# Optimization experiments

Measured on AMD Instinct MI355X. Metric: run time of the kernel, lower is better.

The kernel has to match this reference:

```python
import jax, jax.numpy as jnp
import numpy as np

B, N, C = 2, 2048, 2048
H, KV = 16, 4          # query heads, kv heads
D = C // H             # head_dim = 128
ROPE_BASE = 10000.0


def rope_cos_sin(position_ids, dim):
    # interleaved RoPE: freqs for even indices, repeated pairwise to full dim
    inv_freq = 1.0 / (ROPE_BASE ** (jnp.arange(0, dim, 2, dtype=jnp.float32) / dim))
    ang = position_ids[..., None].astype(jnp.float32) * inv_freq   # [B, N, D/2]
    cos = jnp.repeat(jnp.cos(ang), 2, axis=-1)                     # [B, N, D]
    sin = jnp.repeat(jnp.sin(ang), 2, axis=-1)
    return cos, sin


def rotate_half_interleaved(x):
    # (x0, x1, x2, x3, ...) -> (-x1, x0, -x3, x2, ...)
    x1 = x[..., 0::2]
    x2 = x[..., 1::2]
    return jnp.stack([-x2, x1], axis=-1).reshape(x.shape)


def apply_rotary(x, cos, sin):
    # x: [B, h, N, D]; cos/sin: [B, N, D]
    return x * cos[:, None] + rotate_half_interleaved(x) * sin[:, None]


def setup_inputs() -> dict:
    key = jax.random.key(0)
    ks = jax.random.split(key, 5)
    s = 0.02
    return dict(
        x=jax.random.normal(ks[0], (B, N, C), jnp.float32),
        position_ids=jnp.tile(jnp.arange(N, dtype=jnp.int32), (B, 1)),
        Wq=jax.random.normal(ks[1], (C, C), jnp.float32) * s,
        bq=jnp.zeros((C,), jnp.float32),
        Wk=jax.random.normal(ks[2], (C, KV * D), jnp.float32) * s,
        bk=jnp.zeros((KV * D,), jnp.float32),
        Wv=jax.random.normal(ks[3], (C, KV * D), jnp.float32) * s,
        bv=jnp.zeros((KV * D,), jnp.float32),
        Wo=jax.random.normal(ks[4], (C, C), jnp.float32) * s,
    )


def reference(x, position_ids, Wq, bq, Wk, bk, Wv, bv, Wo):
    Bx, Nx, Cx = x.shape
    q = (x @ Wq + bq).reshape(Bx, Nx, H, D).transpose(0, 2, 1, 3)   # [B,H,N,D]
    k = (x @ Wk + bk).reshape(Bx, Nx, KV, D).transpose(0, 2, 1, 3)  # [B,KV,N,D]
    v = (x @ Wv + bv).reshape(Bx, Nx, KV, D).transpose(0, 2, 1, 3)

    cos, sin = rope_cos_sin(position_ids, D)
    q = apply_rotary(q, cos, sin)
    k = apply_rotary(k, cos, sin)

    # GQA expand: head h uses kv head h // groups (matches unsqueeze+expand+reshape)
    groups = H // KV
    k = jnp.repeat(k, groups, axis=1)   # [B,H,N,D]
    v = jnp.repeat(v, groups, axis=1)

    attn = jnp.einsum('bhqd,bhkd->bhqk', q, k) * (D ** -0.5)        # [B,H,N,N]
    causal_mask = jnp.triu(jnp.ones((Nx, Nx), dtype=bool), 1)
    attn = jnp.where(causal_mask, -jnp.inf, attn)
    attn = jax.nn.softmax(attn, axis=-1)

    out = jnp.einsum('bhqk,bhkd->bhqd', attn, v)
    out = out.transpose(0, 2, 1, 3).reshape(Bx, Nx, Cx)
    return out @ Wo
```

## Files before the change

kernel.cpp:

```cpp
#include <hip/hip_runtime.h>
#include <cstdint>
#include <type_traits>

typedef unsigned short u16;
typedef unsigned int u32;
typedef __bf16 bf16x8 __attribute__((ext_vector_type(8)));
typedef float f32x4 __attribute__((ext_vector_type(4)));

constexpr int BB = 2;
constexpr int SEQ = 2048;
constexpr int CH = 2048;
constexpr int NH = 16;
constexpr int NKV = 4;
constexpr int HD = 128;
constexpr int QKVC = CH + 2 * NKV * HD;

#define DI __device__ __forceinline__

DI u16 f2b(float x) {
  u32 u = __float_as_uint(x);
  u = u + 0x7FFFu + ((u >> 16) & 1u);
  return (u16)(u >> 16);
}
DI float b2f(u16 u) { return __uint_as_float(((u32)u) << 16); }

DI u32 pack2bf(float lo, float hi) {
  return __builtin_amdgcn_perm(__float_as_uint(hi), __float_as_uint(lo), 0x07060302u);
}

DI void glds16(const void* g, void* l) {
  __builtin_amdgcn_global_load_lds(
      (__attribute__((address_space(1))) void*)(uintptr_t)g,
      (__attribute__((address_space(3))) void*)(u32)(uintptr_t)l, 16, 0, 0);
}

__global__ __launch_bounds__(256) void xconv_kernel(const float* __restrict__ in,
                                                    u16* __restrict__ out, int n4) {
  int i = blockIdx.x * 256 + threadIdx.x;
  if (i < n4) {
    float4 v = *(const float4*)&in[(size_t)i * 4];
    ushort4 o;
    o.x = f2b(v.x); o.y = f2b(v.y); o.z = f2b(v.z); o.w = f2b(v.w);
    *(ushort4*)&out[(size_t)i * 4] = o;
  }
}

__global__ __launch_bounds__(256) void wtrans4_kernel(
    const float* __restrict__ Wq, const float* __restrict__ Wk,
    const float* __restrict__ Wv, const float* __restrict__ Wo,
    u16* __restrict__ wqkvt, u16* __restrict__ wot) {
  const int z = blockIdx.z;
  const float* in;
  u16* out;
  int Cc;
  if (z == 0)      { in = Wq; out = wqkvt;                                Cc = CH; }
  else if (z == 1) { in = Wk; out = wqkvt + (size_t)CH * CH;              Cc = NKV * HD; }
  else if (z == 2) { in = Wv; out = wqkvt + (size_t)(CH + NKV * HD) * CH; Cc = NKV * HD; }
  else             { in = Wo; out = wot;                                  Cc = CH; }
  if ((int)blockIdx.y * 64 >= Cc) return;

  __shared__ u16 tile[64 * 65];
  const int r0 = blockIdx.x * 64, c0 = blockIdx.y * 64;
  const int tid = threadIdx.x;
  for (int c = tid; c < 1024; c += 256) {
    int r = c >> 4, col = (c & 15) * 4;
    float4 v = *(const float4*)&in[(size_t)(r0 + r) * Cc + c0 + col];
    tile[r * 65 + col + 0] = f2b(v.x);
    tile[r * 65 + col + 1] = f2b(v.y);
    tile[r * 65 + col + 2] = f2b(v.z);
    tile[r * 65 + col + 3] = f2b(v.w);
  }
  __syncthreads();
  for (int c = tid; c < 1024; c += 256) {
    int r = c >> 4, col = (c & 15) * 4;
    ushort4 v;
    v.x = tile[(col + 0) * 65 + r];
    v.y = tile[(col + 1) * 65 + r];
    v.z = tile[(col + 2) * 65 + r];
    v.w = tile[(col + 3) * 65 + r];
    *(ushort4*)&out[(size_t)(c0 + r) * CH + r0 + col] = v;
  }
}

__global__ __launch_bounds__(256) void vtrans_kernel(const u16* __restrict__ in,
                                                     u16* __restrict__ out) {
  __shared__ u16 tile[64 * 65];
  const int s = blockIdx.z, n0 = blockIdx.x * 64, d0 = blockIdx.y * 64;
  const int tid = threadIdx.x;
  const u16* ip = in + (size_t)s * SEQ * HD + (size_t)n0 * HD + d0;
  u16* op = out + (size_t)s * HD * SEQ + (size_t)d0 * SEQ + n0;
  for (int c = tid; c < 1024; c += 256) {
    int r = c >> 4, col = (c & 15) * 4;
    ushort4 v = *(const ushort4*)&ip[(size_t)r * HD + col];
    tile[r * 65 + col + 0] = v.x;
    tile[r * 65 + col + 1] = v.y;
    tile[r * 65 + col + 2] = v.z;
    tile[r * 65 + col + 3] = v.w;
  }
  __syncthreads();
  for (int c = tid; c < 1024; c += 256) {
    int r = c >> 4, col = (c & 15) * 4;
    ushort4 v;
    v.x = tile[(col + 0) * 65 + r];
    v.y = tile[(col + 1) * 65 + r];
    v.z = tile[(col + 2) * 65 + r];
    v.w = tile[(col + 3) * 65 + r];
    int u = col;
    int w = (u & 3) | (((u >> 5) & 1) << 2) | (((u >> 2) & 3) << 3) | (((u >> 4) & 1) << 5);
    int glp = (w >> 3) ^ (r & 7);
    int colp = glp * 8 + (w & 7);
    *(ushort4*)&op[(size_t)r * SEQ + colp] = v;
  }
}

template <int MODE>
__global__ __launch_bounds__(256, 3) void gemm_kernel(
    const u16* __restrict__ A, const u16* __restrict__ Bt,
    u16* __restrict__ Cb, float* __restrict__ Cf, u16* __restrict__ Vn,
    const float* __restrict__ bq, const float* __restrict__ bk,
    const float* __restrict__ bv, int M, int Nn, int K) {
  __shared__ u16 As[128 * 32];
  __shared__ u16 Bs[128 * 32];
  const int tid = threadIdx.x;
  const int lane = tid & 63, wave = tid >> 6;
  const int wrow = wave >> 1, wcol = wave & 1;
  const int m0 = blockIdx.x * 128, n0 = blockIdx.y * 128;
  const int lm = lane & 15, lq = lane >> 4;
  f32x4 acc[4][4] = {};

  const u16* ag = A + (size_t)(m0 + (tid >> 2)) * K + (tid & 3) * 8;
  const u16* bg = Bt + (size_t)(n0 + (tid >> 2)) * K + (tid & 3) * 8;
  char* asb = (char*)As + wave * 1024;
  char* bsb = (char*)Bs + wave * 1024;
  const size_t rowskip = (size_t)64 * K;

  for (int k = 0; k < K; k += 32) {
    __syncthreads();
    glds16(ag + k, asb);
    glds16(ag + rowskip + k, asb + 4096);
    glds16(bg + k, bsb);
    glds16(bg + rowskip + k, bsb + 4096);
    __syncthreads();
    bf16x8 af[4], bfr[4];
#pragma unroll
    for (int i = 0; i < 4; i++)
      af[i] = *(const bf16x8*)&As[(wrow * 64 + i * 16 + lm) * 32 + lq * 8];
#pragma unroll
    for (int j = 0; j < 4; j++)
      bfr[j] = *(const bf16x8*)&Bs[(wcol * 64 + j * 16 + lm) * 32 + lq * 8];
#pragma unroll
    for (int i = 0; i < 4; i++)
#pragma unroll
      for (int j = 0; j < 4; j++)
        acc[i][j] = __builtin_amdgcn_mfma_f32_16x16x32_bf16(af[i], bfr[j], acc[i][j], 0, 0, 0);
  }

#pragma unroll
  for (int i = 0; i < 4; i++) {
    const int mg = m0 + wrow * 64 + i * 16 + lq * 4;
#pragma unroll
    for (int j = 0; j < 4; j++) {
      const int ng = n0 + wcol * 64 + j * 16 + lm;
      float bias = 0.f;
      if (MODE == 0)
        bias = (ng < CH) ? bq[ng] : (ng < CH + NKV * HD ? bk[ng - CH] : bv[ng - CH - NKV * HD]);
#pragma unroll
      for (int r = 0; r < 4; r++) {
        float v = acc[i][j][r] + bias;
        if (MODE == 0) {
          if (ng >= CH + NKV * HD) {
            int tok = mg + r;
            int bidx = tok >> 11, n = tok & (SEQ - 1);
            int vcol = ng - (CH + NKV * HD);
            int kh = vcol >> 7, d = vcol & (HD - 1);
            Vn[((size_t)(bidx * NKV + kh) * SEQ + n) * HD + d] = f2b(v);
          } else {
            Cb[(size_t)(mg + r) * Nn + ng] = f2b(v);
          }
        } else {
          Cf[(size_t)(mg + r) * Nn + ng] = v;
        }
      }
    }
  }
}

__global__ __launch_bounds__(256) void rope_kernel(
    const u16* __restrict__ qkv, const int* __restrict__ pos,
    u16* __restrict__ Qo, u16* __restrict__ Ko) {
  __shared__ float cs_s[64], sn_s[64];
  const int tok = blockIdx.x;
  const int b = tok >> 11, n = tok & (SEQ - 1);
  const int t = threadIdx.x;
  const u16* row = qkv + (size_t)tok * QKVC;
  const float LN1E4_64 = 0.14391156831212788f;

  if (t < 64) {
    float ang = (float)pos[tok] * expf(-(float)t * LN1E4_64);
    float sn, cs;
    sincosf(ang, &sn, &cs);
    cs_s[t] = cs;
    sn_s[t] = sn;
  }
  __syncthreads();

  for (int idx = t; idx < NH * 64; idx += 256) {
    int hh = idx >> 6, i = idx & 63;
    float cs = cs_s[i], sn = sn_s[i];
    float q0v = b2f(row[hh * 128 + 2 * i]);
    float q1v = b2f(row[hh * 128 + 2 * i + 1]);
    size_t off = ((size_t)(b * NH + hh) * SEQ + n) * HD + 2 * i;
    Qo[off] = f2b(q0v * cs - q1v * sn);
    Qo[off + 1] = f2b(q1v * cs + q0v * sn);
  }
  {
    int kh = t >> 6, i = t & 63;
    float cs = cs_s[i], sn = sn_s[i];
    float k0v = b2f(row[CH + kh * 128 + 2 * i]);
    float k1v = b2f(row[CH + kh * 128 + 2 * i + 1]);
    int d0 = 2 * i;
    int g = d0 >> 3;
    int gp = (g & 8) | ((g ^ n) & 7);
    int dp = gp * 8 + (d0 & 7);
    size_t off = ((size_t)(b * NKV + kh) * SEQ + n) * HD + dp;
    Ko[off] = f2b(k0v * cs - k1v * sn);
    Ko[off + 1] = f2b(k1v * cs + k0v * sn);
  }
}

__global__ __launch_bounds__(256, 2) void flash_kernel(
    const u16* __restrict__ Q, const u16* __restrict__ Kk,
    const u16* __restrict__ Vt, u16* __restrict__ Oo) {
  __shared__ u16 Kb[2][64 * 128];
  __shared__ u16 Vb[2][144 * 64];
  const int tid = threadIdx.x, lane = tid & 63, wave = tid >> 6;
  const int lm = lane & 15, lq = lane >> 4;
  const int p = blockIdx.x;
  const int h = blockIdx.y, b = blockIdx.z;
  const int q0A = p * 64, q0B = (31 - p) * 64;
  const int kvh = h >> 2;
  const u16* Qg = Q + (size_t)(b * NH + h) * SEQ * HD;
  const u16* Kg = Kk + (size_t)(b * NKV + kvh) * SEQ * HD;
  const u16* Vg = Vt + (size_t)(b * NKV + kvh) * HD * SEQ;

  if (tid < 128) Vb[tid >> 6][128 * 64 + (tid & 63)] = 0x3F80;

  bf16x8 qf[2][4];
#pragma unroll
  for (int qg = 0; qg < 2; qg++) {
    const int q0g = qg ? q0B : q0A;
    const u16* qrow = Qg + (size_t)(q0g + wave * 16 + lm) * HD;
#pragma unroll
    for (int kd = 0; kd < 4; kd++)
      qf[qg][kd] = *(const bf16x8*)&qrow[kd * 32 + lq * 8];
  }

  f32x4 oacc[2][8] = {};
  f32x4 oaccS[2] = {};
  const float SCL2 = 0.12754325f;
  const int nIter = 32 - p;

  auto stage = [&](int kv0, int bufi) {
    const char* kb = (const char*)(Kg + (size_t)kv0 * HD);
    char* kl = (char*)&Kb[bufi][0];
    const char* vbb = (const char*)(Vg + (size_t)kv0);
    char* vl = (char*)&Vb[bufi][0];
#pragma unroll
    for (int c = 0; c < 4; c++) {
      int ch = wave * 4 + c;
      glds16(kb + ch * 1024 + lane * 16, kl + ch * 1024);
      glds16(vbb + (size_t)(ch * 8 + (lane >> 3)) * (SEQ * 2) + (lane & 7) * 16,
             vl + ch * 1024);
    }
  };

  stage(0, 0);

  for (int t = 0; t < nIter; t++) {
    __syncthreads();
    if (t + 1 < nIter) stage((t + 1) * 64, (t + 1) & 1);
    const u16* Ks = &Kb[t & 1][0];
    const u16* Vs = &Vb[t & 1][0];
    const int kv0 = t * 64;
    const bool actA = (t <= p);

    auto run = [&](auto dualc) {
      constexpr bool DUAL = decltype(dualc)::value;
      f32x4 sv[2][4] = {};
#pragma unroll
      for (int nt = 0; nt < 4; nt++)
#pragma unroll
        for (int kd = 0; kd < 4; kd++) {
          int g = kd * 4 + lq;
          int gpp = (g & 8) | ((g ^ lm) & 7);
          bf16x8 kf = *(const bf16x8*)&Ks[(nt * 16 + lm) * 128 + gpp * 8];
          sv[1][nt] = __builtin_amdgcn_mfma_f32_16x16x32_bf16(kf, qf[1][kd], sv[1][nt], 0, 0, 0);
          if constexpr (DUAL)
            sv[0][nt] = __builtin_amdgcn_mfma_f32_16x16x32_bf16(kf, qf[0][kd], sv[0][nt], 0, 0, 0);
        }

      alignas(16) u32 pad[2][2][4];
      auto softmax = [&](int qg, int q0g) {
        const int base = q0g + wave * 16;
        if (kv0 + 63 > base) {
          const int qrow = base + lm;
#pragma unroll
          for (int nt = 0; nt < 4; nt++) {
            float pv[4];
#pragma unroll
            for (int r = 0; r < 4; r++) {
              int kvg = kv0 + nt * 16 + lq * 4 + r;
              float e = exp2f(sv[qg][nt][r] * SCL2);
              pv[r] = (kvg > qrow) ? 0.f : e;
            }
            pad[qg][nt & 1][(nt >> 1) * 2 + 0] = pack2bf(pv[0], pv[1]);
            pad[qg][nt & 1][(nt >> 1) * 2 + 1] = pack2bf(pv[2], pv[3]);
          }
        } else {
#pragma unroll
          for (int nt = 0; nt < 4; nt++) {
            float pv[4];
#pragma unroll
            for (int r = 0; r < 4; r++) pv[r] = exp2f(sv[qg][nt][r] * SCL2);
            pad[qg][nt & 1][(nt >> 1) * 2 + 0] = pack2bf(pv[0], pv[1]);
            pad[qg][nt & 1][(nt >> 1) * 2 + 1] = pack2bf(pv[2], pv[3]);
          }
        }
      };
      softmax(1, q0B);
      if constexpr (DUAL) softmax(0, q0A);

#pragma unroll
      for (int ks = 0; ks < 2; ks++) {
        const int glp = (ks * 4 + lq) ^ (lm & 7);
        const bf16x8 pa1 = *(const bf16x8*)&pad[1][ks][0];
        const bf16x8 pa0 = *(const bf16x8*)&pad[0][ks][0];
#pragma unroll
        for (int dt = 0; dt < 8; dt++) {
          bf16x8 vf = *(const bf16x8*)&Vs[(dt * 16 + lm) * 64 + glp * 8];
          oacc[1][dt] = __builtin_amdgcn_mfma_f32_16x16x32_bf16(pa1, vf, oacc[1][dt], 0, 0, 0);
          if constexpr (DUAL)
            oacc[0][dt] = __builtin_amdgcn_mfma_f32_16x16x32_bf16(pa0, vf, oacc[0][dt], 0, 0, 0);
        }
        bf16x8 vf8 = *(const bf16x8*)&Vs[(128 + lm) * 64 + glp * 8];
        oaccS[1] = __builtin_amdgcn_mfma_f32_16x16x32_bf16(pa1, vf8, oaccS[1], 0, 0, 0);
        if constexpr (DUAL)
          oaccS[0] = __builtin_amdgcn_mfma_f32_16x16x32_bf16(pa0, vf8, oaccS[0], 0, 0, 0);
      }
    };
    if (actA) run(std::integral_constant<bool, true>{});
    else      run(std::integral_constant<bool, false>{});
  }

  u16* orow = Oo + (size_t)b * SEQ * CH + (size_t)h * HD;
#pragma unroll
  for (int qg = 0; qg < 2; qg++) {
    const int q0g = qg ? q0B : q0A;
    float inv[4];
#pragma unroll
    for (int r = 0; r < 4; r++) inv[r] = 1.0f / __shfl(oaccS[qg][r], lq * 16);
    const int qrow_base = q0g + wave * 16 + lq * 4;
#pragma unroll
    for (int dt = 0; dt < 8; dt++)
#pragma unroll
      for (int r = 0; r < 4; r++)
        orow[(size_t)(qrow_base + r) * CH + dt * 16 + lm] = f2b(oacc[qg][dt][r] * inv[r]);
  }
}

extern "C" void kernel_launch(void* const* d_in, const int* in_sizes, int n_in,
                              void* d_out, int out_size, void* d_ws, size_t ws_size,
                              hipStream_t stream) {
  const float* x = (const float*)d_in[0];
  const int* pos = (const int*)d_in[1];
  const float* Wq = (const float*)d_in[2];
  const float* bq = (const float*)d_in[3];
  const float* Wk = (const float*)d_in[4];
  const float* bk = (const float*)d_in[5];
  const float* Wv = (const float*)d_in[6];
  const float* bv = (const float*)d_in[7];
  const float* Wo = (const float*)d_in[8];
  float* out = (float*)d_out;

  char* ws = (char*)d_ws;
  u16* xb = (u16*)ws;    ws += (size_t)BB * SEQ * CH * 2;
  u16* wqkvt = (u16*)ws; ws += (size_t)QKVC * CH * 2;
  u16* wot = (u16*)ws;   ws += (size_t)CH * CH * 2;
  u16* qkv = (u16*)ws;   ws += (size_t)BB * SEQ * QKVC * 2;
  u16* qr = (u16*)ws;    ws += (size_t)BB * NH * SEQ * HD * 2;
  u16* kr = (u16*)ws;    ws += (size_t)BB * NKV * SEQ * HD * 2;
  u16* vn = (u16*)ws;    ws += (size_t)BB * NKV * SEQ * HD * 2;
  u16* vt = (u16*)ws;    ws += (size_t)BB * NKV * SEQ * HD * 2;
  u16* ao = (u16*)ws;    ws += (size_t)BB * SEQ * CH * 2;

  xconv_kernel<<<dim3(BB * SEQ * CH / 1024), 256, 0, stream>>>(x, xb, BB * SEQ * CH / 4);
  wtrans4_kernel<<<dim3(32, 32, 4), 256, 0, stream>>>(Wq, Wk, Wv, Wo, wqkvt, wot);
  gemm_kernel<0><<<dim3(32, 24), 256, 0, stream>>>(xb, wqkvt, qkv, (float*)nullptr, vn,
                                                   bq, bk, bv, BB * SEQ, QKVC, CH);
  rope_kernel<<<dim3(BB * SEQ), 256, 0, stream>>>(qkv, pos, qr, kr);
  vtrans_kernel<<<dim3(SEQ / 64, HD / 64, BB * NKV), 256, 0, stream>>>(vn, vt);
  flash_kernel<<<dim3(16, NH, BB), 256, 0, stream>>>(qr, kr, vt, ao);
  gemm_kernel<1><<<dim3(32, 16), 256, 0, stream>>>(ao, wot, (u16*)nullptr, out, nullptr,
                                                   nullptr, nullptr, nullptr, BB * SEQ, CH, CH);
}
```

Before: 312.6 us.

## Process four query tiles per flash block and double GEMM K-tile with swizzle

The flash kernel now gives each block four balanced query tiles instead of two, so every staged K/V tile is reused across more query rows, and the grid is halved. The GEMM K-step doubles from 32 to 64, with an XOR-swizzled LDS layout to avoid bank conflicts, which halves the number of barriers per K. The flash change costs many more registers (launch bounds lowered to 1) and leaves only about one block per CU, which may hurt latency hiding.

```diff
diff --git a/kernel.cpp b/kernel.cpp
--- a/kernel.cpp
+++ b/kernel.cpp
@@ -119,8 +119,8 @@
     u16* __restrict__ Cb, float* __restrict__ Cf, u16* __restrict__ Vn,
     const float* __restrict__ bq, const float* __restrict__ bk,
     const float* __restrict__ bv, int M, int Nn, int K) {
-  __shared__ u16 As[128 * 32];
-  __shared__ u16 Bs[128 * 32];
+  __shared__ u16 As[128 * 64];
+  __shared__ u16 Bs[128 * 64];
   const int tid = threadIdx.x;
   const int lane = tid & 63, wave = tid >> 6;
   const int wrow = wave >> 1, wcol = wave & 1;
@@ -128,31 +128,38 @@
   const int lm = lane & 15, lq = lane >> 4;
   f32x4 acc[4][4] = {};
 
-  const u16* ag = A + (size_t)(m0 + (tid >> 2)) * K + (tid & 3) * 8;
-  const u16* bg = Bt + (size_t)(n0 + (tid >> 2)) * K + (tid & 3) * 8;
+  const int grow = tid >> 3;
+  const int gcol = ((lane & 7) ^ (lane >> 3)) * 8;
+  const u16* ag = A + (size_t)(m0 + grow) * K + gcol;
+  const u16* bg = Bt + (size_t)(n0 + grow) * K + gcol;
   char* asb = (char*)As + wave * 1024;
   char* bsb = (char*)Bs + wave * 1024;
-  const size_t rowskip = (size_t)64 * K;
-
-  for (int k = 0; k < K; k += 32) {
+  const size_t rowskip = (size_t)32 * K;
+
+  for (int k = 0; k < K; k += 64) {
     __syncthreads();
-    glds16(ag + k, asb);
-    glds16(ag + rowskip + k, asb + 4096);
-    glds16(bg + k, bsb);
-    glds16(bg + rowskip + k, bsb + 4096);
+#pragma unroll
+    for (int c = 0; c < 4; c++) {
+      glds16(ag + c * rowskip + k, asb + c * 4096);
+      glds16(bg + c * rowskip + k, bsb + c * 4096);
+    }
     __syncthreads();
-    bf16x8 af[4], bfr[4];
-#pragma unroll
-    for (int i = 0; i < 4; i++)
-      af[i] = *(const bf16x8*)&As[(wrow * 64 + i * 16 + lm) * 32 + lq * 8];
-#pragma unroll
-    for (int j = 0; j < 4; j++)
-      bfr[j] = *(const bf16x8*)&Bs[(wcol * 64 + j * 16 + lm) * 32 + lq * 8];
-#pragma unroll
-    for (int i = 0; i < 4; i++)
+#pragma unroll
+    for (int kk = 0; kk < 2; kk++) {
+      bf16x8 af[4], bfr[4];
+      const int slot = ((kk * 4 + lq) ^ (lm & 7)) * 16;
+#pragma unroll
+      for (int i = 0; i < 4; i++)
+        af[i] = *(const bf16x8*)((const char*)As + (wrow * 64 + i * 16 + lm) * 128 + slot);
 #pragma unroll
       for (int j = 0; j < 4; j++)
-        acc[i][j] = __builtin_amdgcn_mfma_f32_16x16x32_bf16(af[i], bfr[j], acc[i][j], 0, 0, 0);
+        bfr[j] = *(const bf16x8*)((const char*)Bs + (wcol * 64 + j * 16 + lm) * 128 + slot);
+#pragma unroll
+      for (int i = 0; i < 4; i++)
+#pragma unroll
+        for (int j = 0; j < 4; j++)
+          acc[i][j] = __builtin_amdgcn_mfma_f32_16x16x32_bf16(af[i], bfr[j], acc[i][j], 0, 0, 0);
+    }
   }
 
 #pragma unroll
@@ -228,7 +235,7 @@
   }
 }
 
-__global__ __launch_bounds__(256, 2) void flash_kernel(
+__global__ __launch_bounds__(256, 1) void flash_kernel(
     const u16* __restrict__ Q, const u16* __restrict__ Kk,
     const u16* __restrict__ Vt, u16* __restrict__ Oo) {
   __shared__ u16 Kb[2][64 * 128];
@@ -237,7 +244,7 @@
   const int lm = lane & 15, lq = lane >> 4;
   const int p = blockIdx.x;
   const int h = blockIdx.y, b = blockIdx.z;
-  const int q0A = p * 64, q0B = (31 - p) * 64;
+  const int q0s[4] = {(31 - p) * 64, (16 + p) * 64, (15 - p) * 64, p * 64};
   const int kvh = h >> 2;
   const u16* Qg = Q + (size_t)(b * NH + h) * SEQ * HD;
   const u16* Kg = Kk + (size_t)(b * NKV + kvh) * SEQ * HD;
@@ -245,18 +252,17 @@
 
   if (tid < 128) Vb[tid >> 6][128 * 64 + (tid & 63)] = 0x3F80;
 
-  bf16x8 qf[2][4];
-#pragma unroll
-  for (int qg = 0; qg < 2; qg++) {
-    const int q0g = qg ? q0B : q0A;
-    const u16* qrow = Qg + (size_t)(q0g + wave * 16 + lm) * HD;
+  bf16x8 qf[4][4];
+#pragma unroll
+  for (int tu = 0; tu < 4; tu++) {
+    const u16* qrow = Qg + (size_t)(q0s[tu] + wave * 16 + lm) * HD;
 #pragma unroll
     for (int kd = 0; kd < 4; kd++)
-      qf[qg][kd] = *(const bf16x8*)&qrow[kd * 32 + lq * 8];
-  }
-
-  f32x4 oacc[2][8] = {};
-  f32x4 oaccS[2] = {};
+      qf[tu][kd] = *(const bf16x8*)&qrow[kd * 32 + lq * 8];
+  }
+
+  f32x4 oacc[4][8] = {};
+  f32x4 oaccS[4] = {};
   const float SCL2 = 0.12754325f;
   const int nIter = 32 - p;
 
@@ -282,11 +288,15 @@
     const u16* Ks = &Kb[t & 1][0];
     const u16* Vs = &Vb[t & 1][0];
     const int kv0 = t * 64;
-    const bool actA = (t <= p);
-
-    auto run = [&](auto dualc) {
-      constexpr bool DUAL = decltype(dualc)::value;
-      f32x4 sv[2][4] = {};
+    const int na = 1 + (t <= 16 + p) + (t <= 15 - p) + (t <= p);
+
+    auto run = [&](auto nc) {
+      constexpr int N = decltype(nc)::value;
+      f32x4 sv[N][4];
+#pragma unroll
+      for (int tu = 0; tu < N; tu++)
+#pragma unroll
+        for (int nt = 0; nt < 4; nt++) sv[tu][nt] = f32x4{0.f, 0.f, 0.f, 0.f};
 #pragma unroll
       for (int nt = 0; nt < 4; nt++)
 #pragma unroll
@@ -294,14 +304,15 @@
           int g = kd * 4 + lq;
           int gpp = (g & 8) | ((g ^ lm) & 7);
           bf16x8 kf = *(const bf16x8*)&Ks[(nt * 16 + lm) * 128 + gpp * 8];
-          sv[1][nt] = __builtin_amdgcn_mfma_f32_16x16x32_bf16(kf, qf[1][kd], sv[1][nt], 0, 0, 0);
-          if constexpr (DUAL)
-            sv[0][nt] = __builtin_amdgcn_mfma_f32_16x16x32_bf16(kf, qf[0][kd], sv[0][nt], 0, 0, 0);
+#pragma unroll
+          for (int tu = 0; tu < N; tu++)
+            sv[tu][nt] = __builtin_amdgcn_mfma_f32_16x16x32_bf16(kf, qf[tu][kd], sv[tu][nt], 0, 0, 0);
         }
 
-      alignas(16) u32 pad[2][2][4];
-      auto softmax = [&](int qg, int q0g) {
-        const int base = q0g + wave * 16;
+      alignas(16) u32 pad[N][2][4];
+#pragma unroll
+      for (int tu = 0; tu < N; tu++) {
+        const int base = q0s[tu] + wave * 16;
         if (kv0 + 63 > base) {
           const int qrow = base + lm;
 #pragma unroll
@@ -310,61 +321,60 @@
 #pragma unroll
             for (int r = 0; r < 4; r++) {
               int kvg = kv0 + nt * 16 + lq * 4 + r;
-              float e = exp2f(sv[qg][nt][r] * SCL2);
+              float e = exp2f(sv[tu][nt][r] * SCL2);
               pv[r] = (kvg > qrow) ? 0.f : e;
             }
-            pad[qg][nt & 1][(nt >> 1) * 2 + 0] = pack2bf(pv[0], pv[1]);
-            pad[qg][nt & 1][(nt >> 1) * 2 + 1] = pack2bf(pv[2], pv[3]);
+            pad[tu][nt & 1][(nt >> 1) * 2 + 0] = pack2bf(pv[0], pv[1]);
+            pad[tu][nt & 1][(nt >> 1) * 2 + 1] = pack2bf(pv[2], pv[3]);
           }
         } else {
 #pragma unroll
           for (int nt = 0; nt < 4; nt++) {
             float pv[4];
 #pragma unroll
-            for (int r = 0; r < 4; r++) pv[r] = exp2f(sv[qg][nt][r] * SCL2);
-            pad[qg][nt & 1][(nt >> 1) * 2 + 0] = pack2bf(pv[0], pv[1]);
-            pad[qg][nt & 1][(nt >> 1) * 2 + 1] = pack2bf(pv[2], pv[3]);
+            for (int r = 0; r < 4; r++) pv[r] = exp2f(sv[tu][nt][r] * SCL2);
+            pad[tu][nt & 1][(nt >> 1) * 2 + 0] = pack2bf(pv[0], pv[1]);
+            pad[tu][nt & 1][(nt >> 1) * 2 + 1] = pack2bf(pv[2], pv[3]);
           }
         }
-      };
-      softmax(1, q0B);
-      if constexpr (DUAL) softmax(0, q0A);
+      }
 
 #pragma unroll
       for (int ks = 0; ks < 2; ks++) {
         const int glp = (ks * 4 + lq) ^ (lm & 7);
-        const bf16x8 pa1 = *(const bf16x8*)&pad[1][ks][0];
-        const bf16x8 pa0 = *(const bf16x8*)&pad[0][ks][0];
 #pragma unroll
         for (int dt = 0; dt < 8; dt++) {
           bf16x8 vf = *(const bf16x8*)&Vs[(dt * 16 + lm) * 64 + glp * 8];
-          oacc[1][dt] = __builtin_amdgcn_mfma_f32_16x16x32_bf16(pa1, vf, oacc[1][dt], 0, 0, 0);
-          if constexpr (DUAL)
-            oacc[0][dt] = __builtin_amdgcn_mfma_f32_16x16x32_bf16(pa0, vf, oacc[0][dt], 0, 0, 0);
+#pragma unroll
+          for (int tu = 0; tu < N; tu++)
+            oacc[tu][dt] = __builtin_amdgcn_mfma_f32_16x16x32_bf16(
+                *(const bf16x8*)&pad[tu][ks][0], vf, oacc[tu][dt], 0, 0, 0);
         }
         bf16x8 vf8 = *(const bf16x8*)&Vs[(128 + lm) * 64 + glp * 8];
-        oaccS[1] = __builtin_amdgcn_mfma_f32_16x16x32_bf16(pa1, vf8, oaccS[1], 0, 0, 0);
-        if constexpr (DUAL)
-          oaccS[0] = __builtin_amdgcn_mfma_f32_16x16x32_bf16(pa0, vf8, oaccS[0], 0, 0, 0);
+#pragma unroll
+        for (int tu = 0; tu < N; tu++)
+          oaccS[tu] = __builtin_amdgcn_mfma_f32_16x16x32_bf16(
+              *(const bf16x8*)&pad[tu][ks][0], vf8, oaccS[tu], 0, 0, 0);
       }
     };
-    if (actA) run(std::integral_constant<bool, true>{});
-    else      run(std::integral_constant<bool, false>{});
+    if (na == 4)      run(std::integral_constant<int, 4>{});
+    else if (na == 3) run(std::integral_constant<int, 3>{});
+    else if (na == 2) run(std::integral_constant<int, 2>{});
+    else              run(std::integral_constant<int, 1>{});
   }
 
   u16* orow = Oo + (size_t)b * SEQ * CH + (size_t)h * HD;
 #pragma unroll
-  for (int qg = 0; qg < 2; qg++) {
-    const int q0g = qg ? q0B : q0A;
+  for (int tu = 0; tu < 4; tu++) {
     float inv[4];
 #pragma unroll
-    for (int r = 0; r < 4; r++) inv[r] = 1.0f / __shfl(oaccS[qg][r], lq * 16);
-    const int qrow_base = q0g + wave * 16 + lq * 4;
+    for (int r = 0; r < 4; r++) inv[r] = 1.0f / __shfl(oaccS[tu][r], lq * 16);
+    const int qrow_base = q0s[tu] + wave * 16 + lq * 4;
 #pragma unroll
     for (int dt = 0; dt < 8; dt++)
 #pragma unroll
       for (int r = 0; r < 4; r++)
-        orow[(size_t)(qrow_base + r) * CH + dt * 16 + lm] = f2b(oacc[qg][dt][r] * inv[r]);
+        orow[(size_t)(qrow_base + r) * CH + dt * 16 + lm] = f2b(oacc[tu][dt][r] * inv[r]);
   }
 }
 
@@ -399,7 +409,7 @@
                                                    bq, bk, bv, BB * SEQ, QKVC, CH);
   rope_kernel<<<dim3(BB * SEQ), 256, 0, stream>>>(qkv, pos, qr, kr);
   vtrans_kernel<<<dim3(SEQ / 64, HD / 64, BB * NKV), 256, 0, stream>>>(vn, vt);
-  flash_kernel<<<dim3(16, NH, BB), 256, 0, stream>>>(qr, kr, vt, ao);
+  flash_kernel<<<dim3(8, NH, BB), 256, 0, stream>>>(qr, kr, vt, ao);
   gemm_kernel<1><<<dim3(32, 16), 256, 0, stream>>>(ao, wot, (u16*)nullptr, out, nullptr,
                                                    nullptr, nullptr, nullptr, BB * SEQ, CH, CH);
 }
```

Result: slower. 430.5 us (+37.7%).
